# Performance work log

Measured on AMD Instinct MI355X. Metric: run time of the kernel, lower is better.

The kernel has to match this reference:

```python
import jax, jax.numpy as jnp
import numpy as np


def setup_inputs() -> dict:
    key = jax.random.key(0)
    ks = jax.random.split(key, 8)
    B, C, H, W = 8, 256, 64, 64
    Cqk = C // 8
    x = jax.random.normal(ks[0], (B, C, H, W), dtype=jnp.float32)
    # 1x1 conv weights, stored as [out_ch, in_ch] (kernel is 1x1)
    Wq = jax.random.normal(ks[1], (Cqk, C), dtype=jnp.float32) * 0.02
    bq = jnp.zeros((Cqk,), dtype=jnp.float32)
    Wk = jax.random.normal(ks[2], (Cqk, C), dtype=jnp.float32) * 0.02
    bk = jnp.zeros((Cqk,), dtype=jnp.float32)
    Wv = jax.random.normal(ks[3], (C, C), dtype=jnp.float32) * 0.02
    bv = jnp.zeros((C,), dtype=jnp.float32)
    # gamma initialized to zero in the module; use small nonzero so grads flow through attention path meaningfully
    gamma = jnp.asarray([0.5], dtype=jnp.float32)
    return {"x": x, "Wq": Wq, "bq": bq, "Wk": Wk, "bk": bk, "Wv": Wv, "bv": bv, "gamma": gamma}


def reference(x, Wq, bq, Wk, bk, Wv, bv, gamma):
    B, C, H, W = x.shape
    N = H * W
    xf = x.reshape(B, C, N)  # [B, C, N]
    # 1x1 convs == channel-wise matmuls
    q = jnp.einsum('oc,bcn->bno', Wq, xf) + bq  # [B, N, Cqk]
    k = jnp.einsum('oc,bcn->bon', Wk, xf) + bk[None, :, None]  # [B, Cqk, N]
    v = jnp.einsum('oc,bcn->bon', Wv, xf) + bv[None, :, None]  # [B, C, N]
    energy = jnp.einsum('bnd,bdm->bnm', q, k)  # [B, N, N], unscaled as in original
    attn = jax.nn.softmax(energy, axis=-1)
    out = jnp.einsum('bcm,bnm->bcn', v, attn)  # out[:, :, n] = sum_m v[:, :, m] * attn[n, m]
    out = out.reshape(B, C, H, W)
    return gamma[0] * out + x
```

## Files before the change

### kernel.cpp

```cpp
#include <hip/hip_runtime.h>
#include <hip/hip_bf16.h>

#define NB 8
#define CH 256
#define NN 4096
#define CQK 32
#define LOG2E 1.4426950408889634f

typedef __attribute__((ext_vector_type(4))) float f32x4;
typedef __attribute__((ext_vector_type(8))) short bf16x8;
typedef unsigned short u16;

static __device__ __forceinline__ u16 f2bf(float f) {
  unsigned int u = __float_as_uint(f);
  unsigned int r = (u + 0x7fffu + ((u >> 16) & 1u)) >> 16;
  return (u16)r;
}

__global__ void prep_weights(const float* __restrict__ Wq, const float* __restrict__ bq,
                             const float* __restrict__ Wk, const float* __restrict__ bk,
                             const float* __restrict__ Wv,
                             u16* __restrict__ Wqkf, u16* __restrict__ Wvf,
                             float* __restrict__ bqk) {
  int i = blockIdx.x * 256 + threadIdx.x;
  int o = i >> 8, c = i & 255;
  int kk = c >> 5, g2 = (c >> 3) & 3, j = c & 7;
  if (o < 64) {
    float wv = (o < 32) ? Wq[o * 256 + c] * LOG2E : Wk[(o - 32) * 256 + c];
    Wqkf[((((o >> 4) * 8 + kk) * 4 + g2) * 16 + (o & 15)) * 8 + j] = f2bf(wv);
  }
  Wvf[((((o >> 4) * 8 + kk) * 4 + g2) * 16 + (o & 15)) * 8 + j] = f2bf(Wv[i]);
  if (i < 64) bqk[i] = (i < 32) ? bq[i] * LOG2E : bk[i - 32];
}

__global__ __launch_bounds__(256, 2) void fused_proj(
    const float* __restrict__ x, const u16* __restrict__ Wqkf,
    const u16* __restrict__ Wvf, const float* __restrict__ bqk,
    const float* __restrict__ bv,
    u16* __restrict__ qbuf, u16* __restrict__ kbuf, u16* __restrict__ vbuf) {
  __shared__ __align__(128) char xt[64 * 512];
  const int b = blockIdx.y, n0 = blockIdx.x * 64;
  const int tid = threadIdx.x, w = tid >> 6, l = tid & 63, g = l >> 4, lr = l & 15;
  const f32x4 fzero = {0.f, 0.f, 0.f, 0.f};

  {
    const int nl = l, cl = w;
    const float* xp = x + (size_t)b * CH * NN + n0 + nl;
    char* xrow = xt + nl * 512;
    const int swz = (nl & 15) << 4;
#pragma unroll
    for (int p = 0; p < 32; ++p) {
      const int c = p * 8 + cl * 2;
      float f0 = xp[(size_t)c * NN], f1 = xp[(size_t)(c + 1) * NN];
      unsigned int pk = (unsigned int)f2bf(f0) | ((unsigned int)f2bf(f1) << 16);
      *(unsigned int*)(xrow + ((c * 2) ^ swz)) = pk;
    }
  }
  __syncthreads();

  const int aswz = lr << 4;

  {
    f32x4 acc[4];
#pragma unroll
    for (int ct = 0; ct < 4; ++ct) acc[ct] = fzero;
#pragma unroll
    for (int kk = 0; kk < 8; ++kk) {
      bf16x8 af = *(const bf16x8*)(xt + (w * 16 + lr) * 512 + ((kk * 64 + g * 16) ^ aswz));
#pragma unroll
      for (int ct = 0; ct < 4; ++ct) {
        bf16x8 bf = *(const bf16x8*)(Wqkf + (size_t)(((ct * 8 + kk) * 4 + g) * 16 + lr) * 8);
        acc[ct] = __builtin_amdgcn_mfma_f32_16x16x32_bf16(af, bf, acc[ct], 0, 0, 0);
      }
    }
#pragma unroll
    for (int ct = 0; ct < 4; ++ct) {
      const int col = ct * 16 + lr;
      const float bc = bqk[col];
#pragma unroll
      for (int r = 0; r < 4; ++r) {
        const int row = n0 + w * 16 + g * 4 + r;
        u16 h = f2bf(acc[ct][r] + bc);
        if (col < 32) qbuf[((size_t)(b * NN + row)) * 32 + col] = h;
        else          kbuf[((size_t)(b * NN + row)) * 32 + (col - 32)] = h;
      }
    }
  }

  {
    f32x4 vacc[4][4];
#pragma unroll
    for (int ct = 0; ct < 4; ++ct)
#pragma unroll
      for (int mt = 0; mt < 4; ++mt) vacc[ct][mt] = fzero;
#pragma unroll
    for (int kk = 0; kk < 8; ++kk) {
      bf16x8 bfm[4];
#pragma unroll
      for (int mt = 0; mt < 4; ++mt)
        bfm[mt] = *(const bf16x8*)(xt + (mt * 16 + lr) * 512 + ((kk * 64 + g * 16) ^ aswz));
#pragma unroll
      for (int ct = 0; ct < 4; ++ct) {
        bf16x8 af = *(const bf16x8*)(Wvf + (size_t)((((w * 4 + ct) * 8 + kk) * 4 + g) * 16 + lr) * 8);
#pragma unroll
        for (int mt = 0; mt < 4; ++mt)
          vacc[ct][mt] = __builtin_amdgcn_mfma_f32_16x16x32_bf16(af, bfm[mt], vacc[ct][mt], 0, 0, 0);
      }
    }
#pragma unroll
    for (int ct = 0; ct < 4; ++ct) {
#pragma unroll
      for (int mt = 0; mt < 4; ++mt) {
        const int m = n0 + mt * 16 + lr;
#pragma unroll
        for (int r = 0; r < 4; ++r) {
          const int ch = w * 64 + ct * 16 + g * 4 + r;
          vbuf[((size_t)(b * 128 + (m >> 5)) * 256 + ch) * 32 + (m & 31)] = f2bf(vacc[ct][mt][r] + bv[ch]);
        }
      }
    }
  }
}

#define KLOAD2(T, sub) (*(const bf16x8*)(kp + (size_t)((((T) & 31) * 128) + (sub) * 16) * 32))
#define VLOAD(mg, ct) (*(const bf16x8*)(vp + (size_t)((mg) & 127) * 8192 + (ct) * 512))

#define EXPP(S, PW, MASK) {                                                                   \
  float e0 = __builtin_amdgcn_exp2f(S[0]);                                                    \
  float e1 = __builtin_amdgcn_exp2f(S[1]);                                                    \
  float e2 = __builtin_amdgcn_exp2f(S[2]);                                                    \
  float e3 = __builtin_amdgcn_exp2f(S[3]);                                                    \
  lsum += (MASK) * ((e0 + e1) + (e2 + e3));                                                   \
  PW.x = __builtin_amdgcn_perm(__float_as_uint(e1) + 0x8000u, __float_as_uint(e0) + 0x8000u, 0x07060302u); \
  PW.y = __builtin_amdgcn_perm(__float_as_uint(e3) + 0x8000u, __float_as_uint(e2) + 0x8000u, 0x07060302u); \
}

#define PBAR() do {                                  \
  __builtin_amdgcn_sched_barrier(0);                 \
  asm volatile("s_waitcnt lgkmcnt(0)");              \
  __builtin_amdgcn_s_barrier();                      \
  __builtin_amdgcn_sched_barrier(0);                 \
} while (0)

#define QK8(K0, K1, K2, K3, K4, K5, K6, K7, MASK) {                                           \
  f32x4 s0 = __builtin_amdgcn_mfma_f32_16x16x32_bf16(K0, qf, fzero, 0, 0, 0);                 \
  f32x4 s1 = __builtin_amdgcn_mfma_f32_16x16x32_bf16(K1, qf, fzero, 0, 0, 0);                 \
  f32x4 s2 = __builtin_amdgcn_mfma_f32_16x16x32_bf16(K2, qf, fzero, 0, 0, 0);                 \
  f32x4 s3 = __builtin_amdgcn_mfma_f32_16x16x32_bf16(K3, qf, fzero, 0, 0, 0);                 \
  f32x4 s4 = __builtin_amdgcn_mfma_f32_16x16x32_bf16(K4, qf, fzero, 0, 0, 0);                 \
  f32x4 s5 = __builtin_amdgcn_mfma_f32_16x16x32_bf16(K5, qf, fzero, 0, 0, 0);                 \
  f32x4 s6 = __builtin_amdgcn_mfma_f32_16x16x32_bf16(K6, qf, fzero, 0, 0, 0);                 \
  f32x4 s7 = __builtin_amdgcn_mfma_f32_16x16x32_bf16(K7, qf, fzero, 0, 0, 0);                 \
  EXPP(s0, pw0, MASK); EXPP(s1, pw1, MASK); EXPP(s2, pw2, MASK); EXPP(s3, pw3, MASK);         \
  EXPP(s4, pw4, MASK); EXPP(s5, pw5, MASK); EXPP(s6, pw6, MASK); EXPP(s7, pw7, MASK);         \
}

#define PWRITE(BUF) {                                                                         \
  char* pl = (char*)Pb + (BUF) * 32768 + prow * 128;                                          \
  *(uint2*)(pl + ((0 * 32 + g * 8) ^ wswz)) = pw0;                                            \
  *(uint2*)(pl + ((1 * 32 + g * 8) ^ wswz)) = pw1;                                            \
  *(uint2*)(pl + ((2 * 32 + g * 8) ^ wswz)) = pw2;                                            \
  *(uint2*)(pl + ((3 * 32 + g * 8) ^ wswz)) = pw3;                                            \
  char* ph = pl + 16384;                                                                      \
  *(uint2*)(ph + ((0 * 32 + g * 8) ^ wswz)) = pw4;                                            \
  *(uint2*)(ph + ((1 * 32 + g * 8) ^ wswz)) = pw5;                                            \
  *(uint2*)(ph + ((2 * 32 + g * 8) ^ wswz)) = pw6;                                            \
  *(uint2*)(ph + ((3 * 32 + g * 8) ^ wswz)) = pw7;                                            \
}

#define PVQ(BUF, QTR, VA, VB) {                                                               \
  const char* prb = (const char*)Pb + (BUF) * 32768 + ((QTR) >> 1) * 16384;                   \
  _Pragma("unroll")                                                                           \
  for (int nt = 0; nt < 8; ++nt) {                                                            \
    const int row = nt * 16 + lr;                                                             \
    const int rs = (row & 7) << 4;                                                            \
    bf16x8 pa = *(const bf16x8*)(prb + row * 128 + ((((QTR) & 1) * 64 + g * 16) ^ rs));       \
    oacc[nt][0] = __builtin_amdgcn_mfma_f32_16x16x32_bf16(VA, pa, oacc[nt][0], 0, 0, 0);      \
    oacc[nt][1] = __builtin_amdgcn_mfma_f32_16x16x32_bf16(VB, pa, oacc[nt][1], 0, 0, 0);      \
  }                                                                                           \
}

__global__ __launch_bounds__(512, 2) void attn_fused(
    const u16* __restrict__ qb, const u16* __restrict__ kbuf,
    const u16* __restrict__ vbuf, const float* __restrict__ x,
    const float* __restrict__ gamma_p, float* __restrict__ out) {
  __shared__ __align__(128) char Pb[2][2][16384];
  __shared__ float lsum_s[128];

  const int b = blockIdx.x;
  const int n0 = blockIdx.y * 128;
  const int tid = threadIdx.x, w = tid >> 6, l = tid & 63, g = l >> 4, lr = l & 15;
  const float gamma0 = gamma_p[0];
  const f32x4 fzero = {0.f, 0.f, 0.f, 0.f};

  bf16x8 qf = *(const bf16x8*)(qb + ((size_t)b * NN + n0 + w * 16 + lr) * 32 + g * 8);

  const u16* kp = kbuf + (size_t)b * (NN * 32) + (size_t)lr * 32 + g * 8;
  const u16* vp = vbuf + (size_t)b * 1048576 + (size_t)(w * 32 + lr) * 32 + g * 8;

  f32x4 oacc[8][2];
#pragma unroll
  for (int nt = 0; nt < 8; ++nt)
#pragma unroll
    for (int ct = 0; ct < 2; ++ct) oacc[nt][ct] = fzero;
  float lsum = 0.f;

  const int prow = w * 16 + lr;
  const int wswz = (prow & 7) << 4;

  bf16x8 kA0 = KLOAD2(0, 0), kA1 = KLOAD2(0, 1), kA2 = KLOAD2(0, 2), kA3 = KLOAD2(0, 3);
  bf16x8 kA4 = KLOAD2(0, 4), kA5 = KLOAD2(0, 5), kA6 = KLOAD2(0, 6), kA7 = KLOAD2(0, 7);
  bf16x8 kB0 = KLOAD2(1, 0), kB1 = KLOAD2(1, 1), kB2 = KLOAD2(1, 2), kB3 = KLOAD2(1, 3);
  bf16x8 kB4 = KLOAD2(1, 4), kB5 = KLOAD2(1, 5), kB6 = KLOAD2(1, 6), kB7 = KLOAD2(1, 7);
  bf16x8 v0, v1, v2, v3, v4, v5, v6, v7;
  uint2 pw0, pw1, pw2, pw3, pw4, pw5, pw6, pw7;
  QK8(kA0, kA1, kA2, kA3, kA4, kA5, kA6, kA7, 1.0f);
  PWRITE(0);

  for (int T2 = 0; T2 < 16; ++T2) {
    {
      const int T = 2 * T2;
      v0 = VLOAD(4 * T, 0); v1 = VLOAD(4 * T, 1);
      v2 = VLOAD(4 * T + 1, 0); v3 = VLOAD(4 * T + 1, 1);
      QK8(kB0, kB1, kB2, kB3, kB4, kB5, kB6, kB7, 1.0f);
      kA0 = KLOAD2(T + 2, 0); kA1 = KLOAD2(T + 2, 1); kA2 = KLOAD2(T + 2, 2); kA3 = KLOAD2(T + 2, 3);
      kA4 = KLOAD2(T + 2, 4); kA5 = KLOAD2(T + 2, 5); kA6 = KLOAD2(T + 2, 6); kA7 = KLOAD2(T + 2, 7);
      PBAR();
      PWRITE(1);
      v4 = VLOAD(4 * T + 2, 0); v5 = VLOAD(4 * T + 2, 1);
      v6 = VLOAD(4 * T + 3, 0); v7 = VLOAD(4 * T + 3, 1);
      __builtin_amdgcn_s_setprio(1);
      PVQ(0, 0, v0, v1);
      PVQ(0, 1, v2, v3);
      PVQ(0, 2, v4, v5);
      PVQ(0, 3, v6, v7);
      __builtin_amdgcn_s_setprio(0);
    }
    {
      const int T = 2 * T2 + 1;
      const float tmask = (T2 < 15) ? 1.0f : 0.0f;
      v0 = VLOAD(4 * T, 0); v1 = VLOAD(4 * T, 1);
      v2 = VLOAD(4 * T + 1, 0); v3 = VLOAD(4 * T + 1, 1);
      QK8(kA0, kA1, kA2, kA3, kA4, kA5, kA6, kA7, tmask);
      kB0 = KLOAD2(T + 2, 0); kB1 = KLOAD2(T + 2, 1); kB2 = KLOAD2(T + 2, 2); kB3 = KLOAD2(T + 2, 3);
      kB4 = KLOAD2(T + 2, 4); kB5 = KLOAD2(T + 2, 5); kB6 = KLOAD2(T + 2, 6); kB7 = KLOAD2(T + 2, 7);
      PBAR();
      PWRITE(0);
      v4 = VLOAD(4 * T + 2, 0); v5 = VLOAD(4 * T + 2, 1);
      v6 = VLOAD(4 * T + 3, 0); v7 = VLOAD(4 * T + 3, 1);
      __builtin_amdgcn_s_setprio(1);
      PVQ(1, 0, v0, v1);
      PVQ(1, 1, v2, v3);
      PVQ(1, 2, v4, v5);
      PVQ(1, 3, v6, v7);
      __builtin_amdgcn_s_setprio(0);
    }
  }

  lsum += __shfl_xor(lsum, 16);
  lsum += __shfl_xor(lsum, 32);
  if (l < 16) lsum_s[w * 16 + lr] = lsum;
  __syncthreads();

  const size_t bbase = (size_t)b * CH * NN;
#pragma unroll
  for (int nt = 0; nt < 8; ++nt) {
    const int q = nt * 16 + lr;
    const float linv = 1.f / lsum_s[q];
    const int n = n0 + q;
#pragma unroll
    for (int ct = 0; ct < 2; ++ct) {
      const int cbase = w * 32 + ct * 16 + g * 4;
#pragma unroll
      for (int r = 0; r < 4; ++r) {
        const size_t off = bbase + (size_t)(cbase + r) * NN + n;
        out[off] = gamma0 * (oacc[nt][ct][r] * linv) + x[off];
      }
    }
  }
}

extern "C" void kernel_launch(void* const* d_in, const int* in_sizes, int n_in,
                              void* d_out, int out_size, void* d_ws, size_t ws_size,
                              hipStream_t stream) {
  const float* x     = (const float*)d_in[0];
  const float* Wq    = (const float*)d_in[1];
  const float* bq    = (const float*)d_in[2];
  const float* Wk    = (const float*)d_in[3];
  const float* bk    = (const float*)d_in[4];
  const float* Wv    = (const float*)d_in[5];
  const float* bv    = (const float*)d_in[6];
  const float* gamma = (const float*)d_in[7];
  float* out = (float*)d_out;

  char* ws = (char*)d_ws;
  u16*   qbuf = (u16*)(ws);
  u16*   kbuf = (u16*)(ws + 2097152);
  u16*   vbuf = (u16*)(ws + 4194304);
  u16*   Wqkf = (u16*)(ws + 20971520);
  u16*   Wvf  = (u16*)(ws + 21004288);
  float* bqk  = (float*)(ws + 21135360);

  prep_weights<<<256, 256, 0, stream>>>(Wq, bq, Wk, bk, Wv, Wqkf, Wvf, bqk);
  fused_proj<<<dim3(64, 8), 256, 0, stream>>>(x, Wqkf, Wvf, bqk, bv, qbuf, kbuf, vbuf);
  attn_fused<<<dim3(8, 32), 512, 0, stream>>>(qbuf, kbuf, vbuf, x, gamma, out);
}
```

Baseline: 115.8 us.

## Interleave QK exp chunks with PV MFMAs and deepen K/V prefetch pipeline

Restructures the attention main loop so QK^T MFMAs and exp/pack for the next tile are interleaved in pairs between the PV MFMA groups, rather than run as one block before the barrier. K tiles are prefetched one step further ahead, and the first V fragments for the next step are loaded at the end of the current step. The s_setprio bracketing is removed. The aim is to overlap transcendental and VALU work with matrix-core work and hide global-load latency, at the cost of more live registers and changed masking of the tail tile.

```diff
diff --git a/kernel.cpp b/kernel.cpp
--- a/kernel.cpp
+++ b/kernel.cpp
@@ -135,25 +135,18 @@
   PW.y = __builtin_amdgcn_perm(__float_as_uint(e3) + 0x8000u, __float_as_uint(e2) + 0x8000u, 0x07060302u); \
 }
 
+#define QK2(KX, KY, PWX, PWY, MASK) {                                                         \
+  f32x4 sx = __builtin_amdgcn_mfma_f32_16x16x32_bf16(KX, qf, fzero, 0, 0, 0);                 \
+  f32x4 sy = __builtin_amdgcn_mfma_f32_16x16x32_bf16(KY, qf, fzero, 0, 0, 0);                 \
+  EXPP(sx, PWX, MASK); EXPP(sy, PWY, MASK);                                                   \
+}
+
 #define PBAR() do {                                  \
   __builtin_amdgcn_sched_barrier(0);                 \
   asm volatile("s_waitcnt lgkmcnt(0)");              \
   __builtin_amdgcn_s_barrier();                      \
   __builtin_amdgcn_sched_barrier(0);                 \
 } while (0)
-
-#define QK8(K0, K1, K2, K3, K4, K5, K6, K7, MASK) {                                           \
-  f32x4 s0 = __builtin_amdgcn_mfma_f32_16x16x32_bf16(K0, qf, fzero, 0, 0, 0);                 \
-  f32x4 s1 = __builtin_amdgcn_mfma_f32_16x16x32_bf16(K1, qf, fzero, 0, 0, 0);                 \
-  f32x4 s2 = __builtin_amdgcn_mfma_f32_16x16x32_bf16(K2, qf, fzero, 0, 0, 0);                 \
-  f32x4 s3 = __builtin_amdgcn_mfma_f32_16x16x32_bf16(K3, qf, fzero, 0, 0, 0);                 \
-  f32x4 s4 = __builtin_amdgcn_mfma_f32_16x16x32_bf16(K4, qf, fzero, 0, 0, 0);                 \
-  f32x4 s5 = __builtin_amdgcn_mfma_f32_16x16x32_bf16(K5, qf, fzero, 0, 0, 0);                 \
-  f32x4 s6 = __builtin_amdgcn_mfma_f32_16x16x32_bf16(K6, qf, fzero, 0, 0, 0);                 \
-  f32x4 s7 = __builtin_amdgcn_mfma_f32_16x16x32_bf16(K7, qf, fzero, 0, 0, 0);                 \
-  EXPP(s0, pw0, MASK); EXPP(s1, pw1, MASK); EXPP(s2, pw2, MASK); EXPP(s3, pw3, MASK);         \
-  EXPP(s4, pw4, MASK); EXPP(s5, pw5, MASK); EXPP(s6, pw6, MASK); EXPP(s7, pw7, MASK);         \
-}
 
 #define PWRITE(BUF) {                                                                         \
   char* pl = (char*)Pb + (BUF) * 32768 + prow * 128;                                          \
@@ -208,52 +201,63 @@
   const int prow = w * 16 + lr;
   const int wswz = (prow & 7) << 4;
 
-  bf16x8 kA0 = KLOAD2(0, 0), kA1 = KLOAD2(0, 1), kA2 = KLOAD2(0, 2), kA3 = KLOAD2(0, 3);
-  bf16x8 kA4 = KLOAD2(0, 4), kA5 = KLOAD2(0, 5), kA6 = KLOAD2(0, 6), kA7 = KLOAD2(0, 7);
-  bf16x8 kB0 = KLOAD2(1, 0), kB1 = KLOAD2(1, 1), kB2 = KLOAD2(1, 2), kB3 = KLOAD2(1, 3);
-  bf16x8 kB4 = KLOAD2(1, 4), kB5 = KLOAD2(1, 5), kB6 = KLOAD2(1, 6), kB7 = KLOAD2(1, 7);
+  bf16x8 kA0, kA1, kA2, kA3, kA4, kA5, kA6, kA7;
+  bf16x8 kB0, kB1, kB2, kB3, kB4, kB5, kB6, kB7;
   bf16x8 v0, v1, v2, v3, v4, v5, v6, v7;
   uint2 pw0, pw1, pw2, pw3, pw4, pw5, pw6, pw7;
-  QK8(kA0, kA1, kA2, kA3, kA4, kA5, kA6, kA7, 1.0f);
+
+  kA0 = KLOAD2(0, 0); kA1 = KLOAD2(0, 1); kA2 = KLOAD2(0, 2); kA3 = KLOAD2(0, 3);
+  kA4 = KLOAD2(0, 4); kA5 = KLOAD2(0, 5); kA6 = KLOAD2(0, 6); kA7 = KLOAD2(0, 7);
+  QK2(kA0, kA1, pw0, pw1, 1.0f); QK2(kA2, kA3, pw2, pw3, 1.0f);
+  QK2(kA4, kA5, pw4, pw5, 1.0f); QK2(kA6, kA7, pw6, pw7, 1.0f);
   PWRITE(0);
+  kA0 = KLOAD2(1, 0); kA1 = KLOAD2(1, 1); kA2 = KLOAD2(1, 2); kA3 = KLOAD2(1, 3);
+  kA4 = KLOAD2(1, 4); kA5 = KLOAD2(1, 5); kA6 = KLOAD2(1, 6); kA7 = KLOAD2(1, 7);
+  QK2(kA0, kA1, pw0, pw1, 1.0f); QK2(kA2, kA3, pw2, pw3, 1.0f);
+  QK2(kA4, kA5, pw4, pw5, 1.0f); QK2(kA6, kA7, pw6, pw7, 1.0f);
+  kA0 = KLOAD2(2, 0); kA1 = KLOAD2(2, 1); kA2 = KLOAD2(2, 2); kA3 = KLOAD2(2, 3);
+  kA4 = KLOAD2(2, 4); kA5 = KLOAD2(2, 5); kA6 = KLOAD2(2, 6); kA7 = KLOAD2(2, 7);
+  v0 = VLOAD(0, 0); v1 = VLOAD(0, 1); v2 = VLOAD(1, 0); v3 = VLOAD(1, 1);
 
   for (int T2 = 0; T2 < 16; ++T2) {
+    const float mk = (T2 < 15) ? 1.0f : 0.0f;
     {
       const int T = 2 * T2;
-      v0 = VLOAD(4 * T, 0); v1 = VLOAD(4 * T, 1);
-      v2 = VLOAD(4 * T + 1, 0); v3 = VLOAD(4 * T + 1, 1);
-      QK8(kB0, kB1, kB2, kB3, kB4, kB5, kB6, kB7, 1.0f);
-      kA0 = KLOAD2(T + 2, 0); kA1 = KLOAD2(T + 2, 1); kA2 = KLOAD2(T + 2, 2); kA3 = KLOAD2(T + 2, 3);
-      kA4 = KLOAD2(T + 2, 4); kA5 = KLOAD2(T + 2, 5); kA6 = KLOAD2(T + 2, 6); kA7 = KLOAD2(T + 2, 7);
       PBAR();
       PWRITE(1);
       v4 = VLOAD(4 * T + 2, 0); v5 = VLOAD(4 * T + 2, 1);
       v6 = VLOAD(4 * T + 3, 0); v7 = VLOAD(4 * T + 3, 1);
-      __builtin_amdgcn_s_setprio(1);
       PVQ(0, 0, v0, v1);
+      QK2(kA0, kA1, pw0, pw1, mk);
       PVQ(0, 1, v2, v3);
+      QK2(kA2, kA3, pw2, pw3, mk);
       PVQ(0, 2, v4, v5);
+      QK2(kA4, kA5, pw4, pw5, mk);
       PVQ(0, 3, v6, v7);
-      __builtin_amdgcn_s_setprio(0);
+      QK2(kA6, kA7, pw6, pw7, mk);
+      kB0 = KLOAD2(T + 3, 0); kB1 = KLOAD2(T + 3, 1); kB2 = KLOAD2(T + 3, 2); kB3 = KLOAD2(T + 3, 3);
+      kB4 = KLOAD2(T + 3, 4); kB5 = KLOAD2(T + 3, 5); kB6 = KLOAD2(T + 3, 6); kB7 = KLOAD2(T + 3, 7);
+      v0 = VLOAD(4 * T + 4, 0); v1 = VLOAD(4 * T + 4, 1);
+      v2 = VLOAD(4 * T + 5, 0); v3 = VLOAD(4 * T + 5, 1);
     }
     {
       const int T = 2 * T2 + 1;
-      const float tmask = (T2 < 15) ? 1.0f : 0.0f;
-      v0 = VLOAD(4 * T, 0); v1 = VLOAD(4 * T, 1);
-      v2 = VLOAD(4 * T + 1, 0); v3 = VLOAD(4 * T + 1, 1);
-      QK8(kA0, kA1, kA2, kA3, kA4, kA5, kA6, kA7, tmask);
-      kB0 = KLOAD2(T + 2, 0); kB1 = KLOAD2(T + 2, 1); kB2 = KLOAD2(T + 2, 2); kB3 = KLOAD2(T + 2, 3);
-      kB4 = KLOAD2(T + 2, 4); kB5 = KLOAD2(T + 2, 5); kB6 = KLOAD2(T + 2, 6); kB7 = KLOAD2(T + 2, 7);
       PBAR();
       PWRITE(0);
       v4 = VLOAD(4 * T + 2, 0); v5 = VLOAD(4 * T + 2, 1);
       v6 = VLOAD(4 * T + 3, 0); v7 = VLOAD(4 * T + 3, 1);
-      __builtin_amdgcn_s_setprio(1);
       PVQ(1, 0, v0, v1);
+      QK2(kB0, kB1, pw0, pw1, mk);
       PVQ(1, 1, v2, v3);
+      QK2(kB2, kB3, pw2, pw3, mk);
       PVQ(1, 2, v4, v5);
+      QK2(kB4, kB5, pw4, pw5, mk);
       PVQ(1, 3, v6, v7);
-      __builtin_amdgcn_s_setprio(0);
+      QK2(kB6, kB7, pw6, pw7, mk);
+      kA0 = KLOAD2(T + 3, 0); kA1 = KLOAD2(T + 3, 1); kA2 = KLOAD2(T + 3, 2); kA3 = KLOAD2(T + 3, 3);
+      kA4 = KLOAD2(T + 3, 4); kA5 = KLOAD2(T + 3, 5); kA6 = KLOAD2(T + 3, 6); kA7 = KLOAD2(T + 3, 7);
+      v0 = VLOAD(4 * T + 4, 0); v1 = VLOAD(4 * T + 4, 1);
+      v2 = VLOAD(4 * T + 5, 0); v3 = VLOAD(4 * T + 5, 1);
     }
   }
 
```

Measured after the change: 122.6 us. +5.9%, slower.
